# Kernel optimization log

Hardware: AMD Instinct MI355X
Metric: run time of the kernel (lower is better)

## Reference

```python
import math
import jax, jax.numpy as jnp
import numpy as np

B, D, COND, H, K, L, BOUND = 262144, 16, 8, 128, 10, 4, 1.0
D2 = math.ceil(D / 2)          # second split (spline-transformed channels) = 8
D1 = D - D2                    # passthrough channels = 8
DOUT = (3 * K + 1) * D2        # subnet output = 248
PMIN = 1e-3                    # BIN_WIDTH_MIN == BIN_HEIGHT_MIN == DELTA_MIN


def setup_inputs() -> dict:
    key = jax.random.key(0)
    ks = jax.random.split(key, 8)
    x = jax.random.normal(ks[0], (B, D), dtype=jnp.float32)
    c = jax.random.normal(ks[1], (B, COND), dtype=jnp.float32)
    din1 = D1 + COND
    W1s = jax.random.normal(ks[2], (L, din1, H), dtype=jnp.float32) * 0.1
    b1s = jnp.zeros((L, H), dtype=jnp.float32)
    Whs = jax.random.normal(ks[3], (L, H, H), dtype=jnp.float32) * 0.1
    bhs = jnp.zeros((L, H), dtype=jnp.float32)
    Wos = jax.random.normal(ks[4], (L, H, DOUT), dtype=jnp.float32) * 0.1
    bos = jnp.zeros((L, DOUT), dtype=jnp.float32)
    rng = np.random.default_rng(0)  # permutation_seed = 0
    perms = jnp.asarray(np.stack([rng.permutation(D) for _ in range(L)]), dtype=jnp.int32)
    return {"x": x, "c": c, "W1s": W1s, "b1s": b1s, "Whs": Whs, "bhs": bhs,
            "Wos": Wos, "bos": bos, "perms": perms}


def _softmax_with_min(t, m):
    return m + (1.0 - m * t.shape[-1]) * jax.nn.softmax(t, axis=-1)


def _unpack_theta(theta):
    # theta: [B, D2, 3K+1]
    bw_u, bh_u, ks_u = theta[..., :K], theta[..., K:2 * K], theta[..., 2 * K:]
    bin_w = 2.0 * BOUND * _softmax_with_min(bw_u, PMIN)
    bin_h = 2.0 * BOUND * _softmax_with_min(bh_u, PMIN)
    slopes = PMIN + (1.0 - PMIN) * jax.nn.softplus(ks_u) / math.log(2.0)
    pad = ((0, 0), (0, 0), (1, 0))
    x_knots = jnp.pad(jnp.cumsum(bin_w, axis=-1), pad) - BOUND
    y_knots = jnp.pad(jnp.cumsum(bin_h, axis=-1), pad) - BOUND
    return x_knots, y_knots, bin_w, bin_h, slopes


def _spline_fwd(x2, x_knots, y_knots, bin_w, bin_h, slopes):
    # x2: [B, D2]; knots: [B, D2, K+1]; widths/heights: [B, D2, K]; slopes: [B, D2, K+1]
    bin_idx = jnp.sum(x_knots < x2[..., None], axis=-1) - 1  # searchsorted(left) - 1
    in_bounds = (bin_idx >= 0) & (bin_idx < K)
    ci = jnp.clip(bin_idx, 0, K - 1)
    g = lambda t, i: jnp.take_along_axis(t, i[..., None], axis=-1)[..., 0]
    x1, y1 = g(x_knots, ci), g(y_knots, ci)
    xw, yw = g(bin_w, ci), g(bin_h, ci)
    d1, d2 = g(slopes, ci), g(slopes, ci + 1)
    # safe x so rational-quadratic never produces nan for masked-out lanes
    xs = jnp.where(in_bounds, x2, x1 + 0.5 * xw)
    s = yw / xw
    eta = (xs - x1) / xw
    rev_eta = 1.0 - eta
    err = eta * rev_eta
    y_denom = s + (d1 + d2 - 2.0 * s) * err
    y_rq = y1 + yw * (s * eta ** 2 + d1 * err) / y_denom
    jac_num = s ** 2 * (d2 * eta ** 2 + 2.0 * s * err + d1 * rev_eta ** 2)
    log_jac = jnp.log(jac_num) - 2.0 * jnp.log(y_denom)
    # out-of-bounds: linear extrapolation through the outermost knots
    xl, xr = x_knots[..., 0], x_knots[..., -1]
    yb, yt = y_knots[..., 0], y_knots[..., -1]
    y_lin = (yt - yb) / (xr - xl) * (x2 - xl) + yb
    yx = jnp.where(in_bounds, y_rq, y_lin)
    log_jac = jnp.where(in_bounds, log_jac, 0.0)
    return yx, jnp.sum(log_jac, axis=-1)


def _flow_forward(x, c, W1s, b1s, Whs, bhs, Wos, bos, perms):
    log_jac_det = jnp.zeros((x.shape[0],), dtype=x.dtype)
    for i in range(L):
        x1, x2 = x[:, :D1], x[:, D1:]
        h = jax.nn.relu(jnp.concatenate([x1, c], axis=1) @ W1s[i] + b1s[i])
        h = jax.nn.relu(h @ Whs[i] + bhs[i])
        theta = (h @ Wos[i] + bos[i]).reshape(-1, D2, 3 * K + 1)
        x_knots, y_knots, bin_w, bin_h, slopes = _unpack_theta(theta)
        y2, ljd = _spline_fwd(x2, x_knots, y_knots, bin_w, bin_h, slopes)
        log_jac_det = log_jac_det + ljd
        x_out = jnp.concatenate([x1, y2], axis=1)
        x = jnp.take(x_out, perms[i], axis=1)  # x @ channel_perm.T
    return x, log_jac_det


def reference(x, c, W1s, b1s, Whs, bhs, Wos, bos, perms):
    return _flow_forward(x, c, W1s, b1s, Whs, bhs, Wos, bos, perms)
```

## Files before the change

### kernel.cpp

```cpp
#include <hip/hip_runtime.h>

#define B_N   262144
#define PMIN_F 0.001f
#define LOG2E 1.44269504088896340736f
#define LN2   0.69314718055994530942f

typedef _Float16 half4v __attribute__((ext_vector_type(4)));
typedef _Float16 half8  __attribute__((ext_vector_type(8)));
typedef float    floatx4 __attribute__((ext_vector_type(4)));

__device__ __forceinline__ float fexp2(float x) { return __builtin_amdgcn_exp2f(x); }
__device__ __forceinline__ float flog2(float x) { return __builtin_amdgcn_logf(x); }
__device__ __forceinline__ float frcp (float x) { return __builtin_amdgcn_rcpf(x); }

__global__ __launch_bounds__(64) void prep_kernel(
    const float* __restrict__ W1s, const float* __restrict__ b1s,
    const float* __restrict__ Whs, const float* __restrict__ Wos,
    _Float16* __restrict__ ws)
{
    const int bid   = blockIdx.x;
    const int layer = bid / 104;
    const int r     = bid % 104;
    const int lane  = threadIdx.x;
    const int kg    = lane >> 4;
    const int c     = lane & 15;

    half8 v;
    if (r < 8) {
        const int nt = r, n = nt * 16 + c;
        const float* W1 = W1s + layer * 16 * 128;
        const float* b1 = b1s + layer * 128;
        #pragma unroll
        for (int j = 0; j < 8; ++j) {
            const int k = kg * 8 + j;
            v[j] = (k < 16) ? (_Float16)W1[k * 128 + n]
                 : (k == 16) ? (_Float16)b1[n] : (_Float16)0.f;
        }
    } else if (r < 40) {
        const int f = r - 8, nt = f >> 2, ks = f & 3, n = nt * 16 + c;
        const float* Wh = Whs + layer * 128 * 128;
        #pragma unroll
        for (int j = 0; j < 8; ++j) {
            const int k = ks * 32 + kg * 8 + j;
            v[j] = (_Float16)Wh[k * 128 + n];
        }
    } else {
        const int f = r - 40, nt = f >> 2, ks = f & 3, n = nt * 16 + c;
        const int dd = n >> 5, cc = n & 31;
        const float* Wo = Wos + layer * 128 * 248;
        #pragma unroll
        for (int j = 0; j < 8; ++j) {
            const int k = ks * 32 + kg * 8 + j;
            v[j] = (cc < 31) ? (_Float16)Wo[k * 248 + dd * 31 + cc] : (_Float16)0.f;
        }
    }
    *(half8*)(ws + (size_t)bid * 512 + lane * 8) = v;
}

__global__ __launch_bounds__(64, 3) void flow_mfma(
    const float* __restrict__ x_in,
    const float* __restrict__ c_in,
    const float* __restrict__ bhs,
    const float* __restrict__ bos,
    const int*   __restrict__ perms,
    const _Float16* __restrict__ wsW,
    float* __restrict__ out)
{
    __shared__ __align__(16) float    xls[2][256];
    __shared__ __align__(16) _Float16 R[2][2176];

    const int lane = threadIdx.x;
    const int q    = lane >> 4;
    const int m    = lane & 15;
    const long long row0 = (long long)blockIdx.x * 32;

    {
        const float4* xp = (const float4*)(x_in + row0 * 16);
        *(float4*)&xls[0][lane * 4] = xp[lane];
        *(float4*)&xls[1][lane * 4] = xp[lane + 64];
    }

    half8 a1c[2];
    #pragma unroll
    for (int t2 = 0; t2 < 2; ++t2) {
        #pragma unroll
        for (int j = 0; j < 8; ++j) a1c[t2][j] = (_Float16)0.f;
        if (q == 1) {
            const float4* cp = (const float4*)(c_in + (row0 + t2 * 16 + m) * 8);
            const float4 c0 = cp[0], c1 = cp[1];
            a1c[t2][0] = (_Float16)c0.x; a1c[t2][1] = (_Float16)c0.y;
            a1c[t2][2] = (_Float16)c0.z; a1c[t2][3] = (_Float16)c0.w;
            a1c[t2][4] = (_Float16)c1.x; a1c[t2][5] = (_Float16)c1.y;
            a1c[t2][6] = (_Float16)c1.z; a1c[t2][7] = (_Float16)c1.w;
        } else if (q == 2) {
            a1c[t2][0] = (_Float16)1.f;
        }
    }

    const int sp_t2  = lane >> 5;
    const int sp_row = (lane & 31) >> 1;
    const int sp_dl  = lane & 1;

    float ljacc = 0.f;

    for (int l = 0; l < 4; ++l) {
        const _Float16* wsl = wsW + (size_t)l * 104 * 512;
        const float* bh = bhs + l * 128;
        const float* bo = bos + l * 248;

        half8 a1[2];
        #pragma unroll
        for (int t2 = 0; t2 < 2; ++t2) {
            a1[t2] = a1c[t2];
            if (q == 0) {
                const float4 lo = *(const float4*)&xls[t2][m * 16];
                const float4 hi = *(const float4*)&xls[t2][m * 16 + 4];
                a1[t2][0] = (_Float16)lo.x; a1[t2][1] = (_Float16)lo.y;
                a1[t2][2] = (_Float16)lo.z; a1[t2][3] = (_Float16)lo.w;
                a1[t2][4] = (_Float16)hi.x; a1[t2][5] = (_Float16)hi.y;
                a1[t2][6] = (_Float16)hi.z; a1[t2][7] = (_Float16)hi.w;
            }
        }
        #pragma unroll
        for (int g = 0; g < 2; ++g) {
            const floatx4 z = {0.f, 0.f, 0.f, 0.f};
            floatx4 acc0[4], acc1[4];
            #pragma unroll
            for (int nt = 0; nt < 4; ++nt) {
                const half8 b = *(const half8*)(wsl + (g * 4 + nt) * 512 + lane * 8);
                acc0[nt] = __builtin_amdgcn_mfma_f32_16x16x32_f16(a1[0], b, z, 0, 0, 0);
                acc1[nt] = __builtin_amdgcn_mfma_f32_16x16x32_f16(a1[1], b, z, 0, 0, 0);
            }
            #pragma unroll
            for (int nt = 0; nt < 4; ++nt)
                #pragma unroll
                for (int reg = 0; reg < 4; ++reg) {
                    R[0][(q * 4 + reg) * 132 + (g * 4 + nt) * 16 + m] = (_Float16)fmaxf(acc0[nt][reg], 0.f);
                    R[1][(q * 4 + reg) * 132 + (g * 4 + nt) * 16 + m] = (_Float16)fmaxf(acc1[nt][reg], 0.f);
                }
        }

        half8 a2[2][4];
        #pragma unroll
        for (int t2 = 0; t2 < 2; ++t2)
            #pragma unroll
            for (int ks = 0; ks < 4; ++ks) {
                const half4v lo = *(const half4v*)&R[t2][m * 132 + ks * 32 + q * 8];
                const half4v hi = *(const half4v*)&R[t2][m * 132 + ks * 32 + q * 8 + 4];
                a2[t2][ks] = __builtin_shufflevector(lo, hi, 0, 1, 2, 3, 4, 5, 6, 7);
            }
        #pragma unroll
        for (int g = 0; g < 2; ++g) {
            floatx4 acc0[4], acc1[4];
            #pragma unroll
            for (int nt = 0; nt < 4; ++nt) {
                const float bb = bh[(g * 4 + nt) * 16 + m];
                acc0[nt][0] = bb; acc0[nt][1] = bb; acc0[nt][2] = bb; acc0[nt][3] = bb;
                acc1[nt] = acc0[nt];
            }
            #pragma unroll
            for (int ks = 0; ks < 4; ++ks)
                #pragma unroll
                for (int nt = 0; nt < 4; ++nt) {
                    const half8 b = *(const half8*)(wsl + (8 + (g * 4 + nt) * 4 + ks) * 512 + lane * 8);
                    acc0[nt] = __builtin_amdgcn_mfma_f32_16x16x32_f16(a2[0][ks], b, acc0[nt], 0, 0, 0);
                    acc1[nt] = __builtin_amdgcn_mfma_f32_16x16x32_f16(a2[1][ks], b, acc1[nt], 0, 0, 0);
                }
            #pragma unroll
            for (int nt = 0; nt < 4; ++nt)
                #pragma unroll
                for (int reg = 0; reg < 4; ++reg) {
                    R[0][(q * 4 + reg) * 132 + (g * 4 + nt) * 16 + m] = (_Float16)fmaxf(acc0[nt][reg], 0.f);
                    R[1][(q * 4 + reg) * 132 + (g * 4 + nt) * 16 + m] = (_Float16)fmaxf(acc1[nt][reg], 0.f);
                }
        }

        half8 a3[2][4];
        #pragma unroll
        for (int t2 = 0; t2 < 2; ++t2)
            #pragma unroll
            for (int ks = 0; ks < 4; ++ks) {
                const half4v lo = *(const half4v*)&R[t2][m * 132 + ks * 32 + q * 8];
                const half4v hi = *(const half4v*)&R[t2][m * 132 + ks * 32 + q * 8 + 4];
                a3[t2][ks] = __builtin_shufflevector(lo, hi, 0, 1, 2, 3, 4, 5, 6, 7);
            }
        __syncthreads();

        float* Rf0 = (float*)&R[0][0];
        float* Rf1 = (float*)&R[1][0];

        #pragma unroll
        for (int qd = 0; qd < 4; ++qd) {
            {
                floatx4 acc0[4], acc1[4];
                #pragma unroll
                for (int j = 0; j < 4; ++j) {
                    const int n = qd * 64 + j * 16 + m;
                    const int cc = n & 31;
                    const float bb = (cc < 31) ? bo[(n >> 5) * 31 + cc] : 0.f;
                    acc0[j][0] = bb; acc0[j][1] = bb; acc0[j][2] = bb; acc0[j][3] = bb;
                    acc1[j] = acc0[j];
                }
                #pragma unroll
                for (int ks = 0; ks < 4; ++ks)
                    #pragma unroll
                    for (int j = 0; j < 4; ++j) {
                        const int nt = qd * 4 + j;
                        const half8 b = *(const half8*)(wsl + (40 + nt * 4 + ks) * 512 + lane * 8);
                        acc0[j] = __builtin_amdgcn_mfma_f32_16x16x32_f16(a3[0][ks], b, acc0[j], 0, 0, 0);
                        acc1[j] = __builtin_amdgcn_mfma_f32_16x16x32_f16(a3[1][ks], b, acc1[j], 0, 0, 0);
                    }
                #pragma unroll
                for (int j = 0; j < 4; ++j) {
                    const int off = (j >> 1) * 32 + (j & 1) * 16 + m;
                    #pragma unroll
                    for (int reg = 0; reg < 4; ++reg) {
                        Rf0[(q * 4 + reg) * 68 + off] = acc0[j][reg];
                        Rf1[(q * 4 + reg) * 68 + off] = acc1[j][reg];
                    }
                }
            }

            {
                const int d    = qd * 2 + sp_dl;
                const int base = sp_row * 68 + sp_dl * 32;
                const float* Rf = sp_t2 ? Rf1 : Rf0;

                const float4 v0 = *(const float4*)&Rf[base];
                const float4 v1 = *(const float4*)&Rf[base + 4];
                const float4 v2 = *(const float4*)&Rf[base + 8];
                const float4 v3 = *(const float4*)&Rf[base + 12];
                const float4 v4 = *(const float4*)&Rf[base + 16];
                const float x2 = xls[sp_t2][sp_row * 16 + 8 + d];

                float tw[10] = {v0.x, v0.y, v0.z, v0.w, v1.x, v1.y, v1.z, v1.w, v2.x, v2.y};
                float m1 = tw[0];
                #pragma unroll
                for (int i = 1; i < 10; ++i) m1 = fmaxf(m1, tw[i]);
                float se = 0.f;
                #pragma unroll
                for (int i = 0; i < 10; ++i) { tw[i] = fexp2((tw[i] - m1) * LOG2E); se += tw[i]; }
                const float inv198 = 1.98f * frcp(se);

                int cnt = 0;
                {
                    float run = -1.f;
                    cnt += (run < x2) ? 1 : 0;
                    #pragma unroll
                    for (int i = 0; i < 10; ++i) {
                        run = run + fmaf(tw[i], inv198, 0.002f);
                        cnt += (run < x2) ? 1 : 0;
                    }
                }
                const int bidx = cnt - 1;
                const bool inb = (bidx >= 0) && (bidx < 10);
                const int ci = bidx < 0 ? 0 : (bidx > 9 ? 9 : bidx);

                float xlo = -1.f, xhi = 0.f, rx;
                {
                    float run = -1.f;
                    #pragma unroll
                    for (int i = 0; i < 10; ++i) {
                        const bool pick = (i == ci);
                        xlo = pick ? run : xlo;
                        run = run + fmaf(tw[i], inv198, 0.002f);
                        xhi = pick ? run : xhi;
                    }
                    rx = run;
                }

                float hh[10] = {v2.z, v2.w, v3.x, v3.y, v3.z, v3.w, v4.x, v4.y, v4.z, v4.w};
                float hm = hh[0];
                #pragma unroll
                for (int i = 1; i < 10; ++i) hm = fmaxf(hm, hh[i]);
                float seh = 0.f;
                #pragma unroll
                for (int i = 0; i < 10; ++i) { hh[i] = fexp2((hh[i] - hm) * LOG2E); seh += hh[i]; }
                const float invh = 1.98f * frcp(seh);
                float ylo = -1.f, yhi = 0.f, ry;
                {
                    float run = -1.f;
                    #pragma unroll
                    for (int i = 0; i < 10; ++i) {
                        const bool pick = (i == ci);
                        ylo = pick ? run : ylo;
                        run = run + fmaf(hh[i], invh, 0.002f);
                        yhi = pick ? run : yhi;
                    }
                    ry = run;
                }

                const float xw = xhi - xlo, yw = yhi - ylo;

                const float u1 = Rf[base + 20 + ci];
                const float u2 = Rf[base + 21 + ci];
                const float t1 = u1 * LOG2E;
                const float t2s = u2 * LOG2E;
                const float dd1 = PMIN_F + 0.999f * ((t1  > 15.f) ? t1  : flog2(1.f + fexp2(t1)));
                const float dd2 = PMIN_F + 0.999f * ((t2s > 15.f) ? t2s : flog2(1.f + fexp2(t2s)));

                const float xs  = inb ? x2 : (xlo + 0.5f * xw);
                const float rxw = frcp(xw);
                const float s   = yw * rxw;
                const float eta = (xs - xlo) * rxw;
                const float rev = 1.f - eta;
                const float er  = eta * rev;
                const float dn  = s + (dd1 + dd2 - 2.f * s) * er;
                const float yrq = ylo + yw * (s * eta * eta + dd1 * er) * frcp(dn);
                const float jn  = s * s * (dd2 * eta * eta + 2.f * s * er + dd1 * rev * rev);
                const float ljx = LN2 * (flog2(jn) - 2.f * flog2(dn));
                const float ylin = (ry + 1.f) * frcp(rx + 1.f) * (x2 + 1.f) - 1.f;

                xls[sp_t2][sp_row * 16 + 8 + d] = inb ? yrq : ylin;
                ljacc += inb ? ljx : 0.f;
            }
        }

        {
            const int4 pv = ((const int4*)(perms + l * 16))[lane & 3];
            const int mm = lane >> 2;
            const float a0 = xls[0][mm * 16 + pv.x];
            const float a1v = xls[0][mm * 16 + pv.y];
            const float a2v = xls[0][mm * 16 + pv.z];
            const float a3v = xls[0][mm * 16 + pv.w];
            const float b0 = xls[1][mm * 16 + pv.x];
            const float b1v = xls[1][mm * 16 + pv.y];
            const float b2 = xls[1][mm * 16 + pv.z];
            const float b3 = xls[1][mm * 16 + pv.w];
            *(float4*)&xls[0][lane * 4] = make_float4(a0, a1v, a2v, a3v);
            *(float4*)&xls[1][lane * 4] = make_float4(b0, b1v, b2, b3);
        }
        __syncthreads();
    }

    #pragma unroll
    for (int t2 = 0; t2 < 2; ++t2) {
        const float4 vo = *(const float4*)&xls[t2][lane * 4];
        ((float4*)(out + (row0 + t2 * 16) * 16))[lane] = vo;
    }
    {
        const float ljs = ljacc + __shfl_xor(ljacc, 1);
        if ((lane & 1) == 0)
            out[(size_t)B_N * 16 + row0 + sp_t2 * 16 + sp_row] = ljs;
    }
}

extern "C" void kernel_launch(void* const* d_in, const int* in_sizes, int n_in,
                              void* d_out, int out_size, void* d_ws, size_t ws_size,
                              hipStream_t stream) {
    const float* x     = (const float*)d_in[0];
    const float* c     = (const float*)d_in[1];
    const float* W1s   = (const float*)d_in[2];
    const float* b1s   = (const float*)d_in[3];
    const float* Whs   = (const float*)d_in[4];
    const float* bhs   = (const float*)d_in[5];
    const float* Wos   = (const float*)d_in[6];
    const float* bos   = (const float*)d_in[7];
    const int*   perms = (const int*)d_in[8];
    float* out = (float*)d_out;
    _Float16* ws = (_Float16*)d_ws;

    prep_kernel<<<dim3(416), dim3(64), 0, stream>>>(W1s, b1s, Whs, Wos, ws);
    flow_mfma<<<dim3(B_N / 32), dim3(64), 0, stream>>>(
        x, c, bhs, bos, perms, ws, out);
}
```

Baseline: 280.4 us.

## Process 64 rows per wavefront to reuse weight fragments across four M-tiles

Each single-wave block now handles four 16-row tiles instead of two, so every weight B-fragment loaded from global memory feeds four MFMAs rather than two. This halves the weight-load traffic per row and the grid size. The spline evaluation moves into a helper and each lane runs it twice per quarter. In exchange, accumulator and A-fragment register use roughly doubles, so launch bounds drop to two waves per SIMD and shared memory per block doubles, which lowers occupancy and the ability to hide latency.

```diff
diff --git a/kernel.cpp b/kernel.cpp
--- a/kernel.cpp
+++ b/kernel.cpp
@@ -57,7 +57,98 @@
     *(half8*)(ws + (size_t)bid * 512 + lane * 8) = v;
 }
 
-__global__ __launch_bounds__(64, 3) void flow_mfma(
+__device__ __forceinline__ void spline_eval(const float* __restrict__ Rf, const int base,
+                                            const float x2, float& yout, float& ljout)
+{
+    const float4 v0 = *(const float4*)&Rf[base];
+    const float4 v1 = *(const float4*)&Rf[base + 4];
+    const float4 v2 = *(const float4*)&Rf[base + 8];
+    const float4 v3 = *(const float4*)&Rf[base + 12];
+    const float4 v4 = *(const float4*)&Rf[base + 16];
+
+    float tw[10] = {v0.x, v0.y, v0.z, v0.w, v1.x, v1.y, v1.z, v1.w, v2.x, v2.y};
+    float m1 = tw[0];
+    #pragma unroll
+    for (int i = 1; i < 10; ++i) m1 = fmaxf(m1, tw[i]);
+    float se = 0.f;
+    #pragma unroll
+    for (int i = 0; i < 10; ++i) { tw[i] = fexp2((tw[i] - m1) * LOG2E); se += tw[i]; }
+    const float inv198 = 1.98f * frcp(se);
+
+    int cnt = 0;
+    {
+        float run = -1.f;
+        cnt += (run < x2) ? 1 : 0;
+        #pragma unroll
+        for (int i = 0; i < 10; ++i) {
+            run = run + fmaf(tw[i], inv198, 0.002f);
+            cnt += (run < x2) ? 1 : 0;
+        }
+    }
+    const int bidx = cnt - 1;
+    const bool inb = (bidx >= 0) && (bidx < 10);
+    const int ci = bidx < 0 ? 0 : (bidx > 9 ? 9 : bidx);
+
+    float xlo = -1.f, xhi = 0.f, rx;
+    {
+        float run = -1.f;
+        #pragma unroll
+        for (int i = 0; i < 10; ++i) {
+            const bool pick = (i == ci);
+            xlo = pick ? run : xlo;
+            run = run + fmaf(tw[i], inv198, 0.002f);
+            xhi = pick ? run : xhi;
+        }
+        rx = run;
+    }
+
+    float hh[10] = {v2.z, v2.w, v3.x, v3.y, v3.z, v3.w, v4.x, v4.y, v4.z, v4.w};
+    float hm = hh[0];
+    #pragma unroll
+    for (int i = 1; i < 10; ++i) hm = fmaxf(hm, hh[i]);
+    float seh = 0.f;
+    #pragma unroll
+    for (int i = 0; i < 10; ++i) { hh[i] = fexp2((hh[i] - hm) * LOG2E); seh += hh[i]; }
+    const float invh = 1.98f * frcp(seh);
+    float ylo = -1.f, yhi = 0.f, ry;
+    {
+        float run = -1.f;
+        #pragma unroll
+        for (int i = 0; i < 10; ++i) {
+            const bool pick = (i == ci);
+            ylo = pick ? run : ylo;
+            run = run + fmaf(hh[i], invh, 0.002f);
+            yhi = pick ? run : yhi;
+        }
+        ry = run;
+    }
+
+    const float xw = xhi - xlo, yw = yhi - ylo;
+
+    const float u1 = Rf[base + 20 + ci];
+    const float u2 = Rf[base + 21 + ci];
+    const float t1 = u1 * LOG2E;
+    const float t2s = u2 * LOG2E;
+    const float dd1 = PMIN_F + 0.999f * ((t1  > 15.f) ? t1  : flog2(1.f + fexp2(t1)));
+    const float dd2 = PMIN_F + 0.999f * ((t2s > 15.f) ? t2s : flog2(1.f + fexp2(t2s)));
+
+    const float xs  = inb ? x2 : (xlo + 0.5f * xw);
+    const float rxw = frcp(xw);
+    const float s   = yw * rxw;
+    const float eta = (xs - xlo) * rxw;
+    const float rev = 1.f - eta;
+    const float er  = eta * rev;
+    const float dn  = s + (dd1 + dd2 - 2.f * s) * er;
+    const float yrq = ylo + yw * (s * eta * eta + dd1 * er) * frcp(dn);
+    const float jn  = s * s * (dd2 * eta * eta + 2.f * s * er + dd1 * rev * rev);
+    const float ljx = LN2 * (flog2(jn) - 2.f * flog2(dn));
+    const float ylin = (ry + 1.f) * frcp(rx + 1.f) * (x2 + 1.f) - 1.f;
+
+    yout  = inb ? yrq : ylin;
+    ljout = inb ? ljx : 0.f;
+}
+
+__global__ __launch_bounds__(64, 2) void flow_mfma(
     const float* __restrict__ x_in,
     const float* __restrict__ c_in,
     const float* __restrict__ bhs,
@@ -66,140 +157,148 @@
     const _Float16* __restrict__ wsW,
     float* __restrict__ out)
 {
-    __shared__ __align__(16) float    xls[2][256];
-    __shared__ __align__(16) _Float16 R[2][2176];
+    __shared__ __align__(16) float    xls[4][256];
+    __shared__ __align__(16) _Float16 R[4][2176];
 
     const int lane = threadIdx.x;
     const int q    = lane >> 4;
     const int m    = lane & 15;
-    const long long row0 = (long long)blockIdx.x * 32;
+    const long long row0 = (long long)blockIdx.x * 64;
 
     {
         const float4* xp = (const float4*)(x_in + row0 * 16);
-        *(float4*)&xls[0][lane * 4] = xp[lane];
-        *(float4*)&xls[1][lane * 4] = xp[lane + 64];
-    }
-
-    half8 a1c[2];
-    #pragma unroll
-    for (int t2 = 0; t2 < 2; ++t2) {
-        #pragma unroll
-        for (int j = 0; j < 8; ++j) a1c[t2][j] = (_Float16)0.f;
+        #pragma unroll
+        for (int t = 0; t < 4; ++t)
+            *(float4*)&xls[t][lane * 4] = xp[lane + t * 64];
+    }
+
+    half8 a1c[4];
+    #pragma unroll
+    for (int t = 0; t < 4; ++t) {
+        #pragma unroll
+        for (int j = 0; j < 8; ++j) a1c[t][j] = (_Float16)0.f;
         if (q == 1) {
-            const float4* cp = (const float4*)(c_in + (row0 + t2 * 16 + m) * 8);
+            const float4* cp = (const float4*)(c_in + (row0 + t * 16 + m) * 8);
             const float4 c0 = cp[0], c1 = cp[1];
-            a1c[t2][0] = (_Float16)c0.x; a1c[t2][1] = (_Float16)c0.y;
-            a1c[t2][2] = (_Float16)c0.z; a1c[t2][3] = (_Float16)c0.w;
-            a1c[t2][4] = (_Float16)c1.x; a1c[t2][5] = (_Float16)c1.y;
-            a1c[t2][6] = (_Float16)c1.z; a1c[t2][7] = (_Float16)c1.w;
+            a1c[t][0] = (_Float16)c0.x; a1c[t][1] = (_Float16)c0.y;
+            a1c[t][2] = (_Float16)c0.z; a1c[t][3] = (_Float16)c0.w;
+            a1c[t][4] = (_Float16)c1.x; a1c[t][5] = (_Float16)c1.y;
+            a1c[t][6] = (_Float16)c1.z; a1c[t][7] = (_Float16)c1.w;
         } else if (q == 2) {
-            a1c[t2][0] = (_Float16)1.f;
-        }
-    }
-
-    const int sp_t2  = lane >> 5;
+            a1c[t][0] = (_Float16)1.f;
+        }
+    }
+
+    const int sp_ta  = lane >> 5;
     const int sp_row = (lane & 31) >> 1;
     const int sp_dl  = lane & 1;
 
-    float ljacc = 0.f;
+    float ljA = 0.f, ljB = 0.f;
 
     for (int l = 0; l < 4; ++l) {
         const _Float16* wsl = wsW + (size_t)l * 104 * 512;
         const float* bh = bhs + l * 128;
         const float* bo = bos + l * 248;
 
-        half8 a1[2];
-        #pragma unroll
-        for (int t2 = 0; t2 < 2; ++t2) {
-            a1[t2] = a1c[t2];
+        half8 a1[4];
+        #pragma unroll
+        for (int t = 0; t < 4; ++t) {
+            a1[t] = a1c[t];
             if (q == 0) {
-                const float4 lo = *(const float4*)&xls[t2][m * 16];
-                const float4 hi = *(const float4*)&xls[t2][m * 16 + 4];
-                a1[t2][0] = (_Float16)lo.x; a1[t2][1] = (_Float16)lo.y;
-                a1[t2][2] = (_Float16)lo.z; a1[t2][3] = (_Float16)lo.w;
-                a1[t2][4] = (_Float16)hi.x; a1[t2][5] = (_Float16)hi.y;
-                a1[t2][6] = (_Float16)hi.z; a1[t2][7] = (_Float16)hi.w;
+                const float4 lo = *(const float4*)&xls[t][m * 16];
+                const float4 hi = *(const float4*)&xls[t][m * 16 + 4];
+                a1[t][0] = (_Float16)lo.x; a1[t][1] = (_Float16)lo.y;
+                a1[t][2] = (_Float16)lo.z; a1[t][3] = (_Float16)lo.w;
+                a1[t][4] = (_Float16)hi.x; a1[t][5] = (_Float16)hi.y;
+                a1[t][6] = (_Float16)hi.z; a1[t][7] = (_Float16)hi.w;
             }
         }
         #pragma unroll
         for (int g = 0; g < 2; ++g) {
             const floatx4 z = {0.f, 0.f, 0.f, 0.f};
-            floatx4 acc0[4], acc1[4];
+            floatx4 acc[4][4];
             #pragma unroll
             for (int nt = 0; nt < 4; ++nt) {
                 const half8 b = *(const half8*)(wsl + (g * 4 + nt) * 512 + lane * 8);
-                acc0[nt] = __builtin_amdgcn_mfma_f32_16x16x32_f16(a1[0], b, z, 0, 0, 0);
-                acc1[nt] = __builtin_amdgcn_mfma_f32_16x16x32_f16(a1[1], b, z, 0, 0, 0);
+                #pragma unroll
+                for (int t = 0; t < 4; ++t)
+                    acc[t][nt] = __builtin_amdgcn_mfma_f32_16x16x32_f16(a1[t], b, z, 0, 0, 0);
             }
             #pragma unroll
             for (int nt = 0; nt < 4; ++nt)
                 #pragma unroll
-                for (int reg = 0; reg < 4; ++reg) {
-                    R[0][(q * 4 + reg) * 132 + (g * 4 + nt) * 16 + m] = (_Float16)fmaxf(acc0[nt][reg], 0.f);
-                    R[1][(q * 4 + reg) * 132 + (g * 4 + nt) * 16 + m] = (_Float16)fmaxf(acc1[nt][reg], 0.f);
-                }
-        }
-
-        half8 a2[2][4];
-        #pragma unroll
-        for (int t2 = 0; t2 < 2; ++t2)
+                for (int reg = 0; reg < 4; ++reg)
+                    #pragma unroll
+                    for (int t = 0; t < 4; ++t)
+                        R[t][(q * 4 + reg) * 132 + (g * 4 + nt) * 16 + m] =
+                            (_Float16)fmaxf(acc[t][nt][reg], 0.f);
+        }
+
+        half8 a2[4][4];
+        #pragma unroll
+        for (int t = 0; t < 4; ++t)
             #pragma unroll
             for (int ks = 0; ks < 4; ++ks) {
-                const half4v lo = *(const half4v*)&R[t2][m * 132 + ks * 32 + q * 8];
-                const half4v hi = *(const half4v*)&R[t2][m * 132 + ks * 32 + q * 8 + 4];
-                a2[t2][ks] = __builtin_shufflevector(lo, hi, 0, 1, 2, 3, 4, 5, 6, 7);
+                const half4v lo = *(const half4v*)&R[t][m * 132 + ks * 32 + q * 8];
+                const half4v hi = *(const half4v*)&R[t][m * 132 + ks * 32 + q * 8 + 4];
+                a2[t][ks] = __builtin_shufflevector(lo, hi, 0, 1, 2, 3, 4, 5, 6, 7);
             }
         #pragma unroll
         for (int g = 0; g < 2; ++g) {
-            floatx4 acc0[4], acc1[4];
+            floatx4 acc[4][4];
             #pragma unroll
             for (int nt = 0; nt < 4; ++nt) {
                 const float bb = bh[(g * 4 + nt) * 16 + m];
-                acc0[nt][0] = bb; acc0[nt][1] = bb; acc0[nt][2] = bb; acc0[nt][3] = bb;
-                acc1[nt] = acc0[nt];
+                #pragma unroll
+                for (int t = 0; t < 4; ++t) {
+                    acc[t][nt][0] = bb; acc[t][nt][1] = bb;
+                    acc[t][nt][2] = bb; acc[t][nt][3] = bb;
+                }
             }
             #pragma unroll
             for (int ks = 0; ks < 4; ++ks)
                 #pragma unroll
                 for (int nt = 0; nt < 4; ++nt) {
                     const half8 b = *(const half8*)(wsl + (8 + (g * 4 + nt) * 4 + ks) * 512 + lane * 8);
-                    acc0[nt] = __builtin_amdgcn_mfma_f32_16x16x32_f16(a2[0][ks], b, acc0[nt], 0, 0, 0);
-                    acc1[nt] = __builtin_amdgcn_mfma_f32_16x16x32_f16(a2[1][ks], b, acc1[nt], 0, 0, 0);
+                    #pragma unroll
+                    for (int t = 0; t < 4; ++t)
+                        acc[t][nt] = __builtin_amdgcn_mfma_f32_16x16x32_f16(a2[t][ks], b, acc[t][nt], 0, 0, 0);
                 }
             #pragma unroll
             for (int nt = 0; nt < 4; ++nt)
                 #pragma unroll
-                for (int reg = 0; reg < 4; ++reg) {
-                    R[0][(q * 4 + reg) * 132 + (g * 4 + nt) * 16 + m] = (_Float16)fmaxf(acc0[nt][reg], 0.f);
-                    R[1][(q * 4 + reg) * 132 + (g * 4 + nt) * 16 + m] = (_Float16)fmaxf(acc1[nt][reg], 0.f);
-                }
-        }
-
-        half8 a3[2][4];
-        #pragma unroll
-        for (int t2 = 0; t2 < 2; ++t2)
+                for (int reg = 0; reg < 4; ++reg)
+                    #pragma unroll
+                    for (int t = 0; t < 4; ++t)
+                        R[t][(q * 4 + reg) * 132 + (g * 4 + nt) * 16 + m] =
+                            (_Float16)fmaxf(acc[t][nt][reg], 0.f);
+        }
+
+        half8 a3[4][4];
+        #pragma unroll
+        for (int t = 0; t < 4; ++t)
             #pragma unroll
             for (int ks = 0; ks < 4; ++ks) {
-                const half4v lo = *(const half4v*)&R[t2][m * 132 + ks * 32 + q * 8];
-                const half4v hi = *(const half4v*)&R[t2][m * 132 + ks * 32 + q * 8 + 4];
-                a3[t2][ks] = __builtin_shufflevector(lo, hi, 0, 1, 2, 3, 4, 5, 6, 7);
+                const half4v lo = *(const half4v*)&R[t][m * 132 + ks * 32 + q * 8];
+                const half4v hi = *(const half4v*)&R[t][m * 132 + ks * 32 + q * 8 + 4];
+                a3[t][ks] = __builtin_shufflevector(lo, hi, 0, 1, 2, 3, 4, 5, 6, 7);
             }
         __syncthreads();
-
-        float* Rf0 = (float*)&R[0][0];
-        float* Rf1 = (float*)&R[1][0];
 
         #pragma unroll
         for (int qd = 0; qd < 4; ++qd) {
             {
-                floatx4 acc0[4], acc1[4];
+                floatx4 acc[4][4];
                 #pragma unroll
                 for (int j = 0; j < 4; ++j) {
                     const int n = qd * 64 + j * 16 + m;
                     const int cc = n & 31;
                     const float bb = (cc < 31) ? bo[(n >> 5) * 31 + cc] : 0.f;
-                    acc0[j][0] = bb; acc0[j][1] = bb; acc0[j][2] = bb; acc0[j][3] = bb;
-                    acc1[j] = acc0[j];
+                    #pragma unroll
+                    for (int t = 0; t < 4; ++t) {
+                        acc[t][j][0] = bb; acc[t][j][1] = bb;
+                        acc[t][j][2] = bb; acc[t][j][3] = bb;
+                    }
                 }
                 #pragma unroll
                 for (int ks = 0; ks < 4; ++ks)
@@ -207,141 +306,64 @@
                     for (int j = 0; j < 4; ++j) {
                         const int nt = qd * 4 + j;
                         const half8 b = *(const half8*)(wsl + (40 + nt * 4 + ks) * 512 + lane * 8);
-                        acc0[j] = __builtin_amdgcn_mfma_f32_16x16x32_f16(a3[0][ks], b, acc0[j], 0, 0, 0);
-                        acc1[j] = __builtin_amdgcn_mfma_f32_16x16x32_f16(a3[1][ks], b, acc1[j], 0, 0, 0);
+                        #pragma unroll
+                        for (int t = 0; t < 4; ++t)
+                            acc[t][j] = __builtin_amdgcn_mfma_f32_16x16x32_f16(a3[t][ks], b, acc[t][j], 0, 0, 0);
                     }
                 #pragma unroll
                 for (int j = 0; j < 4; ++j) {
                     const int off = (j >> 1) * 32 + (j & 1) * 16 + m;
                     #pragma unroll
-                    for (int reg = 0; reg < 4; ++reg) {
-                        Rf0[(q * 4 + reg) * 68 + off] = acc0[j][reg];
-                        Rf1[(q * 4 + reg) * 68 + off] = acc1[j][reg];
-                    }
+                    for (int reg = 0; reg < 4; ++reg)
+                        #pragma unroll
+                        for (int t = 0; t < 4; ++t)
+                            ((float*)&R[t][0])[(q * 4 + reg) * 68 + off] = acc[t][j][reg];
                 }
             }
 
             {
                 const int d    = qd * 2 + sp_dl;
                 const int base = sp_row * 68 + sp_dl * 32;
-                const float* Rf = sp_t2 ? Rf1 : Rf0;
-
-                const float4 v0 = *(const float4*)&Rf[base];
-                const float4 v1 = *(const float4*)&Rf[base + 4];
-                const float4 v2 = *(const float4*)&Rf[base + 8];
-                const float4 v3 = *(const float4*)&Rf[base + 12];
-                const float4 v4 = *(const float4*)&Rf[base + 16];
-                const float x2 = xls[sp_t2][sp_row * 16 + 8 + d];
-
-                float tw[10] = {v0.x, v0.y, v0.z, v0.w, v1.x, v1.y, v1.z, v1.w, v2.x, v2.y};
-                float m1 = tw[0];
-                #pragma unroll
-                for (int i = 1; i < 10; ++i) m1 = fmaxf(m1, tw[i]);
-                float se = 0.f;
-                #pragma unroll
-                for (int i = 0; i < 10; ++i) { tw[i] = fexp2((tw[i] - m1) * LOG2E); se += tw[i]; }
-                const float inv198 = 1.98f * frcp(se);
-
-                int cnt = 0;
-                {
-                    float run = -1.f;
-                    cnt += (run < x2) ? 1 : 0;
-                    #pragma unroll
-                    for (int i = 0; i < 10; ++i) {
-                        run = run + fmaf(tw[i], inv198, 0.002f);
-                        cnt += (run < x2) ? 1 : 0;
-                    }
-                }
-                const int bidx = cnt - 1;
-                const bool inb = (bidx >= 0) && (bidx < 10);
-                const int ci = bidx < 0 ? 0 : (bidx > 9 ? 9 : bidx);
-
-                float xlo = -1.f, xhi = 0.f, rx;
-                {
-                    float run = -1.f;
-                    #pragma unroll
-                    for (int i = 0; i < 10; ++i) {
-                        const bool pick = (i == ci);
-                        xlo = pick ? run : xlo;
-                        run = run + fmaf(tw[i], inv198, 0.002f);
-                        xhi = pick ? run : xhi;
-                    }
-                    rx = run;
-                }
-
-                float hh[10] = {v2.z, v2.w, v3.x, v3.y, v3.z, v3.w, v4.x, v4.y, v4.z, v4.w};
-                float hm = hh[0];
-                #pragma unroll
-                for (int i = 1; i < 10; ++i) hm = fmaxf(hm, hh[i]);
-                float seh = 0.f;
-                #pragma unroll
-                for (int i = 0; i < 10; ++i) { hh[i] = fexp2((hh[i] - hm) * LOG2E); seh += hh[i]; }
-                const float invh = 1.98f * frcp(seh);
-                float ylo = -1.f, yhi = 0.f, ry;
-                {
-                    float run = -1.f;
-                    #pragma unroll
-                    for (int i = 0; i < 10; ++i) {
-                        const bool pick = (i == ci);
-                        ylo = pick ? run : ylo;
-                        run = run + fmaf(hh[i], invh, 0.002f);
-                        yhi = pick ? run : yhi;
-                    }
-                    ry = run;
-                }
-
-                const float xw = xhi - xlo, yw = yhi - ylo;
-
-                const float u1 = Rf[base + 20 + ci];
-                const float u2 = Rf[base + 21 + ci];
-                const float t1 = u1 * LOG2E;
-                const float t2s = u2 * LOG2E;
-                const float dd1 = PMIN_F + 0.999f * ((t1  > 15.f) ? t1  : flog2(1.f + fexp2(t1)));
-                const float dd2 = PMIN_F + 0.999f * ((t2s > 15.f) ? t2s : flog2(1.f + fexp2(t2s)));
-
-                const float xs  = inb ? x2 : (xlo + 0.5f * xw);
-                const float rxw = frcp(xw);
-                const float s   = yw * rxw;
-                const float eta = (xs - xlo) * rxw;
-                const float rev = 1.f - eta;
-                const float er  = eta * rev;
-                const float dn  = s + (dd1 + dd2 - 2.f * s) * er;
-                const float yrq = ylo + yw * (s * eta * eta + dd1 * er) * frcp(dn);
-                const float jn  = s * s * (dd2 * eta * eta + 2.f * s * er + dd1 * rev * rev);
-                const float ljx = LN2 * (flog2(jn) - 2.f * flog2(dn));
-                const float ylin = (ry + 1.f) * frcp(rx + 1.f) * (x2 + 1.f) - 1.f;
-
-                xls[sp_t2][sp_row * 16 + 8 + d] = inb ? yrq : ylin;
-                ljacc += inb ? ljx : 0.f;
+                const int xi   = sp_row * 16 + 8 + d;
+
+                float yA, lA, yB, lB;
+                spline_eval((const float*)&R[sp_ta][0],     base, xls[sp_ta][xi],     yA, lA);
+                spline_eval((const float*)&R[sp_ta + 2][0], base, xls[sp_ta + 2][xi], yB, lB);
+
+                xls[sp_ta][xi]     = yA;
+                xls[sp_ta + 2][xi] = yB;
+                ljA += lA;
+                ljB += lB;
             }
         }
 
         {
             const int4 pv = ((const int4*)(perms + l * 16))[lane & 3];
             const int mm = lane >> 2;
-            const float a0 = xls[0][mm * 16 + pv.x];
-            const float a1v = xls[0][mm * 16 + pv.y];
-            const float a2v = xls[0][mm * 16 + pv.z];
-            const float a3v = xls[0][mm * 16 + pv.w];
-            const float b0 = xls[1][mm * 16 + pv.x];
-            const float b1v = xls[1][mm * 16 + pv.y];
-            const float b2 = xls[1][mm * 16 + pv.z];
-            const float b3 = xls[1][mm * 16 + pv.w];
-            *(float4*)&xls[0][lane * 4] = make_float4(a0, a1v, a2v, a3v);
-            *(float4*)&xls[1][lane * 4] = make_float4(b0, b1v, b2, b3);
+            #pragma unroll
+            for (int t = 0; t < 4; ++t) {
+                const float a0  = xls[t][mm * 16 + pv.x];
+                const float a1v = xls[t][mm * 16 + pv.y];
+                const float a2v = xls[t][mm * 16 + pv.z];
+                const float a3v = xls[t][mm * 16 + pv.w];
+                *(float4*)&xls[t][lane * 4] = make_float4(a0, a1v, a2v, a3v);
+            }
         }
         __syncthreads();
     }
 
     #pragma unroll
-    for (int t2 = 0; t2 < 2; ++t2) {
-        const float4 vo = *(const float4*)&xls[t2][lane * 4];
-        ((float4*)(out + (row0 + t2 * 16) * 16))[lane] = vo;
-    }
-    {
-        const float ljs = ljacc + __shfl_xor(ljacc, 1);
-        if ((lane & 1) == 0)
-            out[(size_t)B_N * 16 + row0 + sp_t2 * 16 + sp_row] = ljs;
+    for (int t = 0; t < 4; ++t) {
+        const float4 vo = *(const float4*)&xls[t][lane * 4];
+        ((float4*)(out + (row0 + t * 16) * 16))[lane] = vo;
+    }
+    {
+        const float sA = ljA + __shfl_xor(ljA, 1);
+        const float sB = ljB + __shfl_xor(ljB, 1);
+        if ((lane & 1) == 0) {
+            out[(size_t)B_N * 16 + row0 + sp_ta * 16 + sp_row]       = sA;
+            out[(size_t)B_N * 16 + row0 + (sp_ta + 2) * 16 + sp_row] = sB;
+        }
     }
 }
 
@@ -361,6 +383,6 @@
     _Float16* ws = (_Float16*)d_ws;
 
     prep_kernel<<<dim3(416), dim3(64), 0, stream>>>(W1s, b1s, Whs, Wos, ws);
-    flow_mfma<<<dim3(B_N / 32), dim3(64), 0, stream>>>(
+    flow_mfma<<<dim3(B_N / 64), dim3(64), 0, stream>>>(
         x, c, bhs, bos, perms, ws, out);
 }
```

After: 346.7 us. +23.6%, slower.

## Cut register pressure to raise occupancy to four waves per EU

Applied to the files above, without the earlier changes.

Replaces launch_bounds min-blocks 3 with amdgpu_waves_per_eu(4) and reduces live registers so more waves fit. The hoisted conditioning-input fragment is now rebuilt from global memory every layer instead of being kept in registers. MFMA loops now process two N-tiles at a time instead of four, so fewer accumulators are live. The spline code moves into a helper that defers the height loads. The aim is more waves to hide latency, at the cost of reloading c each layer and possible spills or lost instruction-level parallelism.

```diff
diff --git a/kernel.cpp b/kernel.cpp
--- a/kernel.cpp
+++ b/kernel.cpp
@@ -57,7 +57,100 @@
     *(half8*)(ws + (size_t)bid * 512 + lane * 8) = v;
 }
 
-__global__ __launch_bounds__(64, 3) void flow_mfma(
+__device__ __forceinline__ void spline_eval(const float* __restrict__ Rf, const int base,
+                                            const float x2, float& yout, float& ljout)
+{
+    const float4 v0 = *(const float4*)&Rf[base];
+    const float4 v1 = *(const float4*)&Rf[base + 4];
+    const float4 v2 = *(const float4*)&Rf[base + 8];
+
+    float tw[10] = {v0.x, v0.y, v0.z, v0.w, v1.x, v1.y, v1.z, v1.w, v2.x, v2.y};
+    float m1 = tw[0];
+    #pragma unroll
+    for (int i = 1; i < 10; ++i) m1 = fmaxf(m1, tw[i]);
+    float se = 0.f;
+    #pragma unroll
+    for (int i = 0; i < 10; ++i) { tw[i] = fexp2((tw[i] - m1) * LOG2E); se += tw[i]; }
+    const float inv198 = 1.98f * frcp(se);
+
+    int cnt = 0;
+    {
+        float run = -1.f;
+        cnt += (run < x2) ? 1 : 0;
+        #pragma unroll
+        for (int i = 0; i < 10; ++i) {
+            run = run + fmaf(tw[i], inv198, 0.002f);
+            cnt += (run < x2) ? 1 : 0;
+        }
+    }
+    const int bidx = cnt - 1;
+    const bool inb = (bidx >= 0) && (bidx < 10);
+    const int ci = bidx < 0 ? 0 : (bidx > 9 ? 9 : bidx);
+
+    float xlo = -1.f, xhi = 0.f, rx;
+    {
+        float run = -1.f;
+        #pragma unroll
+        for (int i = 0; i < 10; ++i) {
+            const bool pick = (i == ci);
+            xlo = pick ? run : xlo;
+            run = run + fmaf(tw[i], inv198, 0.002f);
+            xhi = pick ? run : xhi;
+        }
+        rx = run;
+    }
+
+    const float4 v3 = *(const float4*)&Rf[base + 12];
+    const float4 v4 = *(const float4*)&Rf[base + 16];
+
+    float hh[10] = {v2.z, v2.w, v3.x, v3.y, v3.z, v3.w, v4.x, v4.y, v4.z, v4.w};
+    float hm = hh[0];
+    #pragma unroll
+    for (int i = 1; i < 10; ++i) hm = fmaxf(hm, hh[i]);
+    float seh = 0.f;
+    #pragma unroll
+    for (int i = 0; i < 10; ++i) { hh[i] = fexp2((hh[i] - hm) * LOG2E); seh += hh[i]; }
+    const float invh = 1.98f * frcp(seh);
+    float ylo = -1.f, yhi = 0.f, ry;
+    {
+        float run = -1.f;
+        #pragma unroll
+        for (int i = 0; i < 10; ++i) {
+            const bool pick = (i == ci);
+            ylo = pick ? run : ylo;
+            run = run + fmaf(hh[i], invh, 0.002f);
+            yhi = pick ? run : yhi;
+        }
+        ry = run;
+    }
+
+    const float xw = xhi - xlo, yw = yhi - ylo;
+
+    const float u1 = Rf[base + 20 + ci];
+    const float u2 = Rf[base + 21 + ci];
+    const float t1 = u1 * LOG2E;
+    const float t2s = u2 * LOG2E;
+    const float dd1 = PMIN_F + 0.999f * ((t1  > 15.f) ? t1  : flog2(1.f + fexp2(t1)));
+    const float dd2 = PMIN_F + 0.999f * ((t2s > 15.f) ? t2s : flog2(1.f + fexp2(t2s)));
+
+    const float xs  = inb ? x2 : (xlo + 0.5f * xw);
+    const float rxw = frcp(xw);
+    const float s   = yw * rxw;
+    const float eta = (xs - xlo) * rxw;
+    const float rev = 1.f - eta;
+    const float er  = eta * rev;
+    const float dn  = s + (dd1 + dd2 - 2.f * s) * er;
+    const float yrq = ylo + yw * (s * eta * eta + dd1 * er) * frcp(dn);
+    const float jn  = s * s * (dd2 * eta * eta + 2.f * s * er + dd1 * rev * rev);
+    const float ljx = LN2 * (flog2(jn) - 2.f * flog2(dn));
+    const float ylin = (ry + 1.f) * frcp(rx + 1.f) * (x2 + 1.f) - 1.f;
+
+    yout  = inb ? yrq : ylin;
+    ljout = inb ? ljx : 0.f;
+}
+
+__global__ __attribute__((amdgpu_waves_per_eu(4))) __launch_bounds__(64)
+void flow_mfma(
     const float* __restrict__ x_in,
     const float* __restrict__ c_in,
     const float* __restrict__ bhs,
@@ -80,23 +173,6 @@
         *(float4*)&xls[1][lane * 4] = xp[lane + 64];
     }
 
-    half8 a1c[2];
-    #pragma unroll
-    for (int t2 = 0; t2 < 2; ++t2) {
-        #pragma unroll
-        for (int j = 0; j < 8; ++j) a1c[t2][j] = (_Float16)0.f;
-        if (q == 1) {
-            const float4* cp = (const float4*)(c_in + (row0 + t2 * 16 + m) * 8);
-            const float4 c0 = cp[0], c1 = cp[1];
-            a1c[t2][0] = (_Float16)c0.x; a1c[t2][1] = (_Float16)c0.y;
-            a1c[t2][2] = (_Float16)c0.z; a1c[t2][3] = (_Float16)c0.w;
-            a1c[t2][4] = (_Float16)c1.x; a1c[t2][5] = (_Float16)c1.y;
-            a1c[t2][6] = (_Float16)c1.z; a1c[t2][7] = (_Float16)c1.w;
-        } else if (q == 2) {
-            a1c[t2][0] = (_Float16)1.f;
-        }
-    }
-
     const int sp_t2  = lane >> 5;
     const int sp_row = (lane & 31) >> 1;
     const int sp_dl  = lane & 1;
@@ -111,7 +187,8 @@
         half8 a1[2];
         #pragma unroll
         for (int t2 = 0; t2 < 2; ++t2) {
-            a1[t2] = a1c[t2];
+            #pragma unroll
+            for (int j = 0; j < 8; ++j) a1[t2][j] = (_Float16)0.f;
             if (q == 0) {
                 const float4 lo = *(const float4*)&xls[t2][m * 16];
                 const float4 hi = *(const float4*)&xls[t2][m * 16 + 4];
@@ -119,26 +196,38 @@
                 a1[t2][2] = (_Float16)lo.z; a1[t2][3] = (_Float16)lo.w;
                 a1[t2][4] = (_Float16)hi.x; a1[t2][5] = (_Float16)hi.y;
                 a1[t2][6] = (_Float16)hi.z; a1[t2][7] = (_Float16)hi.w;
-            }
-        }
-        #pragma unroll
-        for (int g = 0; g < 2; ++g) {
-            const floatx4 z = {0.f, 0.f, 0.f, 0.f};
-            floatx4 acc0[4], acc1[4];
-            #pragma unroll
-            for (int nt = 0; nt < 4; ++nt) {
-                const half8 b = *(const half8*)(wsl + (g * 4 + nt) * 512 + lane * 8);
-                acc0[nt] = __builtin_amdgcn_mfma_f32_16x16x32_f16(a1[0], b, z, 0, 0, 0);
-                acc1[nt] = __builtin_amdgcn_mfma_f32_16x16x32_f16(a1[1], b, z, 0, 0, 0);
-            }
-            #pragma unroll
-            for (int nt = 0; nt < 4; ++nt)
+            } else if (q == 1) {
+                const float4* cp = (const float4*)(c_in + (row0 + t2 * 16 + m) * 8);
+                const float4 c0 = cp[0], c1 = cp[1];
+                a1[t2][0] = (_Float16)c0.x; a1[t2][1] = (_Float16)c0.y;
+                a1[t2][2] = (_Float16)c0.z; a1[t2][3] = (_Float16)c0.w;
+                a1[t2][4] = (_Float16)c1.x; a1[t2][5] = (_Float16)c1.y;
+                a1[t2][6] = (_Float16)c1.z; a1[t2][7] = (_Float16)c1.w;
+            } else if (q == 2) {
+                a1[t2][0] = (_Float16)1.f;
+            }
+        }
+
+        #pragma unroll
+        for (int g = 0; g < 2; ++g)
+            #pragma unroll
+            for (int p = 0; p < 2; ++p) {
+                const int nt0 = g * 4 + p * 2, nt1 = nt0 + 1;
+                const floatx4 z = {0.f, 0.f, 0.f, 0.f};
+                const half8 b0 = *(const half8*)(wsl + nt0 * 512 + lane * 8);
+                const half8 b1 = *(const half8*)(wsl + nt1 * 512 + lane * 8);
+                floatx4 acc00 = __builtin_amdgcn_mfma_f32_16x16x32_f16(a1[0], b0, z, 0, 0, 0);
+                floatx4 acc01 = __builtin_amdgcn_mfma_f32_16x16x32_f16(a1[1], b0, z, 0, 0, 0);
+                floatx4 acc10 = __builtin_amdgcn_mfma_f32_16x16x32_f16(a1[0], b1, z, 0, 0, 0);
+                floatx4 acc11 = __builtin_amdgcn_mfma_f32_16x16x32_f16(a1[1], b1, z, 0, 0, 0);
                 #pragma unroll
                 for (int reg = 0; reg < 4; ++reg) {
-                    R[0][(q * 4 + reg) * 132 + (g * 4 + nt) * 16 + m] = (_Float16)fmaxf(acc0[nt][reg], 0.f);
-                    R[1][(q * 4 + reg) * 132 + (g * 4 + nt) * 16 + m] = (_Float16)fmaxf(acc1[nt][reg], 0.f);
-                }
-        }
+                    R[0][(q * 4 + reg) * 132 + nt0 * 16 + m] = (_Float16)fmaxf(acc00[reg], 0.f);
+                    R[1][(q * 4 + reg) * 132 + nt0 * 16 + m] = (_Float16)fmaxf(acc01[reg], 0.f);
+                    R[0][(q * 4 + reg) * 132 + nt1 * 16 + m] = (_Float16)fmaxf(acc10[reg], 0.f);
+                    R[1][(q * 4 + reg) * 132 + nt1 * 16 + m] = (_Float16)fmaxf(acc11[reg], 0.f);
+                }
+            }
 
         half8 a2[2][4];
         #pragma unroll
@@ -149,31 +238,38 @@
                 const half4v hi = *(const half4v*)&R[t2][m * 132 + ks * 32 + q * 8 + 4];
                 a2[t2][ks] = __builtin_shufflevector(lo, hi, 0, 1, 2, 3, 4, 5, 6, 7);
             }
-        #pragma unroll
-        for (int g = 0; g < 2; ++g) {
-            floatx4 acc0[4], acc1[4];
-            #pragma unroll
-            for (int nt = 0; nt < 4; ++nt) {
-                const float bb = bh[(g * 4 + nt) * 16 + m];
-                acc0[nt][0] = bb; acc0[nt][1] = bb; acc0[nt][2] = bb; acc0[nt][3] = bb;
-                acc1[nt] = acc0[nt];
-            }
-            #pragma unroll
-            for (int ks = 0; ks < 4; ++ks)
+
+        #pragma unroll
+        for (int g = 0; g < 2; ++g)
+            #pragma unroll
+            for (int p = 0; p < 2; ++p) {
+                const int nt0 = g * 4 + p * 2, nt1 = nt0 + 1;
+                floatx4 acc00, acc01, acc10, acc11;
+                {
+                    const float bb0 = bh[nt0 * 16 + m];
+                    const float bb1 = bh[nt1 * 16 + m];
+                    acc00[0] = bb0; acc00[1] = bb0; acc00[2] = bb0; acc00[3] = bb0;
+                    acc01 = acc00;
+                    acc10[0] = bb1; acc10[1] = bb1; acc10[2] = bb1; acc10[3] = bb1;
+                    acc11 = acc10;
+                }
                 #pragma unroll
-                for (int nt = 0; nt < 4; ++nt) {
-                    const half8 b = *(const half8*)(wsl + (8 + (g * 4 + nt) * 4 + ks) * 512 + lane * 8);
-                    acc0[nt] = __builtin_amdgcn_mfma_f32_16x16x32_f16(a2[0][ks], b, acc0[nt], 0, 0, 0);
-                    acc1[nt] = __builtin_amdgcn_mfma_f32_16x16x32_f16(a2[1][ks], b, acc1[nt], 0, 0, 0);
-                }
-            #pragma unroll
-            for (int nt = 0; nt < 4; ++nt)
+                for (int ks = 0; ks < 4; ++ks) {
+                    const half8 b0 = *(const half8*)(wsl + (8 + nt0 * 4 + ks) * 512 + lane * 8);
+                    const half8 b1 = *(const half8*)(wsl + (8 + nt1 * 4 + ks) * 512 + lane * 8);
+                    acc00 = __builtin_amdgcn_mfma_f32_16x16x32_f16(a2[0][ks], b0, acc00, 0, 0, 0);
+                    acc01 = __builtin_amdgcn_mfma_f32_16x16x32_f16(a2[1][ks], b0, acc01, 0, 0, 0);
+                    acc10 = __builtin_amdgcn_mfma_f32_16x16x32_f16(a2[0][ks], b1, acc10, 0, 0, 0);
+                    acc11 = __builtin_amdgcn_mfma_f32_16x16x32_f16(a2[1][ks], b1, acc11, 0, 0, 0);
+                }
                 #pragma unroll
                 for (int reg = 0; reg < 4; ++reg) {
-                    R[0][(q * 4 + reg) * 132 + (g * 4 + nt) * 16 + m] = (_Float16)fmaxf(acc0[nt][reg], 0.f);
-                    R[1][(q * 4 + reg) * 132 + (g * 4 + nt) * 16 + m] = (_Float16)fmaxf(acc1[nt][reg], 0.f);
-                }
-        }
+                    R[0][(q * 4 + reg) * 132 + nt0 * 16 + m] = (_Float16)fmaxf(acc00[reg], 0.f);
+                    R[1][(q * 4 + reg) * 132 + nt0 * 16 + m] = (_Float16)fmaxf(acc01[reg], 0.f);
+                    R[0][(q * 4 + reg) * 132 + nt1 * 16 + m] = (_Float16)fmaxf(acc10[reg], 0.f);
+                    R[1][(q * 4 + reg) * 132 + nt1 * 16 + m] = (_Float16)fmaxf(acc11[reg], 0.f);
+                }
+            }
 
         half8 a3[2][4];
         #pragma unroll
@@ -191,32 +287,40 @@
 
         #pragma unroll
         for (int qd = 0; qd < 4; ++qd) {
-            {
-                floatx4 acc0[4], acc1[4];
+            #pragma unroll
+            for (int p = 0; p < 2; ++p) {
+                const int j0 = p * 2, j1 = j0 + 1;
+                floatx4 acc00, acc01, acc10, acc11;
+                {
+                    const int n0 = qd * 64 + j0 * 16 + m;
+                    const int n1 = qd * 64 + j1 * 16 + m;
+                    const int cc0 = n0 & 31, cc1 = n1 & 31;
+                    const float bb0 = (cc0 < 31) ? bo[(n0 >> 5) * 31 + cc0] : 0.f;
+                    const float bb1 = (cc1 < 31) ? bo[(n1 >> 5) * 31 + cc1] : 0.f;
+                    acc00[0] = bb0; acc00[1] = bb0; acc00[2] = bb0; acc00[3] = bb0;
+                    acc01 = acc00;
+                    acc10[0] = bb1; acc10[1] = bb1; acc10[2] = bb1; acc10[3] = bb1;
+                    acc11 = acc10;
+                }
                 #pragma unroll
-                for (int j = 0; j < 4; ++j) {
-                    const int n = qd * 64 + j * 16 + m;
-                    const int cc = n & 31;
-                    const float bb = (cc < 31) ? bo[(n >> 5) * 31 + cc] : 0.f;
-                    acc0[j][0] = bb; acc0[j][1] = bb; acc0[j][2] = bb; acc0[j][3] = bb;
-                    acc1[j] = acc0[j];
-                }
-                #pragma unroll
-                for (int ks = 0; ks < 4; ++ks)
-                    #pragma unroll
-                    for (int j = 0; j < 4; ++j) {
-                        const int nt = qd * 4 + j;
-                        const half8 b = *(const half8*)(wsl + (40 + nt * 4 + ks) * 512 + lane * 8);
-                        acc0[j] = __builtin_amdgcn_mfma_f32_16x16x32_f16(a3[0][ks], b, acc0[j], 0, 0, 0);
-                        acc1[j] = __builtin_amdgcn_mfma_f32_16x16x32_f16(a3[1][ks], b, acc1[j], 0, 0, 0);
-                    }
-                #pragma unroll
-                for (int j = 0; j < 4; ++j) {
-                    const int off = (j >> 1) * 32 + (j & 1) * 16 + m;
+                for (int ks = 0; ks < 4; ++ks) {
+                    const int nt0 = qd * 4 + j0, nt1 = qd * 4 + j1;
+                    const half8 b0 = *(const half8*)(wsl + (40 + nt0 * 4 + ks) * 512 + lane * 8);
+                    const half8 b1 = *(const half8*)(wsl + (40 + nt1 * 4 + ks) * 512 + lane * 8);
+                    acc00 = __builtin_amdgcn_mfma_f32_16x16x32_f16(a3[0][ks], b0, acc00, 0, 0, 0);
+                    acc01 = __builtin_amdgcn_mfma_f32_16x16x32_f16(a3[1][ks], b0, acc01, 0, 0, 0);
+                    acc10 = __builtin_amdgcn_mfma_f32_16x16x32_f16(a3[0][ks], b1, acc10, 0, 0, 0);
+                    acc11 = __builtin_amdgcn_mfma_f32_16x16x32_f16(a3[1][ks], b1, acc11, 0, 0, 0);
+                }
+                {
+                    const int off0 = (j0 >> 1) * 32 + (j0 & 1) * 16 + m;
+                    const int off1 = (j1 >> 1) * 32 + (j1 & 1) * 16 + m;
                     #pragma unroll
                     for (int reg = 0; reg < 4; ++reg) {
-                        Rf0[(q * 4 + reg) * 68 + off] = acc0[j][reg];
-                        Rf1[(q * 4 + reg) * 68 + off] = acc1[j][reg];
+                        Rf0[(q * 4 + reg) * 68 + off0] = acc00[reg];
+                        Rf1[(q * 4 + reg) * 68 + off0] = acc01[reg];
+                        Rf0[(q * 4 + reg) * 68 + off1] = acc10[reg];
+                        Rf1[(q * 4 + reg) * 68 + off1] = acc11[reg];
                     }
                 }
             }
@@ -225,94 +329,12 @@
                 const int d    = qd * 2 + sp_dl;
                 const int base = sp_row * 68 + sp_dl * 32;
                 const float* Rf = sp_t2 ? Rf1 : Rf0;
-
-                const float4 v0 = *(const float4*)&Rf[base];
-                const float4 v1 = *(const float4*)&Rf[base + 4];
-                const float4 v2 = *(const float4*)&Rf[base + 8];
-                const float4 v3 = *(const float4*)&Rf[base + 12];
-                const float4 v4 = *(const float4*)&Rf[base + 16];
-                const float x2 = xls[sp_t2][sp_row * 16 + 8 + d];
-
-                float tw[10] = {v0.x, v0.y, v0.z, v0.w, v1.x, v1.y, v1.z, v1.w, v2.x, v2.y};
-                float m1 = tw[0];
-                #pragma unroll
-                for (int i = 1; i < 10; ++i) m1 = fmaxf(m1, tw[i]);
-                float se = 0.f;
-                #pragma unroll
-                for (int i = 0; i < 10; ++i) { tw[i] = fexp2((tw[i] - m1) * LOG2E); se += tw[i]; }
-                const float inv198 = 1.98f * frcp(se);
-
-                int cnt = 0;
-                {
-                    float run = -1.f;
-                    cnt += (run < x2) ? 1 : 0;
-                    #pragma unroll
-                    for (int i = 0; i < 10; ++i) {
-                        run = run + fmaf(tw[i], inv198, 0.002f);
-                        cnt += (run < x2) ? 1 : 0;
-                    }
-                }
-                const int bidx = cnt - 1;
-                const bool inb = (bidx >= 0) && (bidx < 10);
-                const int ci = bidx < 0 ? 0 : (bidx > 9 ? 9 : bidx);
-
-                float xlo = -1.f, xhi = 0.f, rx;
-                {
-                    float run = -1.f;
-                    #pragma unroll
-                    for (int i = 0; i < 10; ++i) {
-                        const bool pick = (i == ci);
-                        xlo = pick ? run : xlo;
-                        run = run + fmaf(tw[i], inv198, 0.002f);
-                        xhi = pick ? run : xhi;
-                    }
-                    rx = run;
-                }
-
-                float hh[10] = {v2.z, v2.w, v3.x, v3.y, v3.z, v3.w, v4.x, v4.y, v4.z, v4.w};
-                float hm = hh[0];
-                #pragma unroll
-                for (int i = 1; i < 10; ++i) hm = fmaxf(hm, hh[i]);
-                float seh = 0.f;
-                #pragma unroll
-                for (int i = 0; i < 10; ++i) { hh[i] = fexp2((hh[i] - hm) * LOG2E); seh += hh[i]; }
-                const float invh = 1.98f * frcp(seh);
-                float ylo = -1.f, yhi = 0.f, ry;
-                {
-                    float run = -1.f;
-                    #pragma unroll
-                    for (int i = 0; i < 10; ++i) {
-                        const bool pick = (i == ci);
-                        ylo = pick ? run : ylo;
-                        run = run + fmaf(hh[i], invh, 0.002f);
-                        yhi = pick ? run : yhi;
-                    }
-                    ry = run;
-                }
-
-                const float xw = xhi - xlo, yw = yhi - ylo;
-
-                const float u1 = Rf[base + 20 + ci];
-                const float u2 = Rf[base + 21 + ci];
-                const float t1 = u1 * LOG2E;
-                const float t2s = u2 * LOG2E;
-                const float dd1 = PMIN_F + 0.999f * ((t1  > 15.f) ? t1  : flog2(1.f + fexp2(t1)));
-                const float dd2 = PMIN_F + 0.999f * ((t2s > 15.f) ? t2s : flog2(1.f + fexp2(t2s)));
-
-                const float xs  = inb ? x2 : (xlo + 0.5f * xw);
-                const float rxw = frcp(xw);
-                const float s   = yw * rxw;
-                const float eta = (xs - xlo) * rxw;
-                const float rev = 1.f - eta;
-                const float er  = eta * rev;
-                const float dn  = s + (dd1 + dd2 - 2.f * s) * er;
-                const float yrq = ylo + yw * (s * eta * eta + dd1 * er) * frcp(dn);
-                const float jn  = s * s * (dd2 * eta * eta + 2.f * s * er + dd1 * rev * rev);
-                const float ljx = LN2 * (flog2(jn) - 2.f * flog2(dn));
-                const float ylin = (ry + 1.f) * frcp(rx + 1.f) * (x2 + 1.f) - 1.f;
-
-                xls[sp_t2][sp_row * 16 + 8 + d] = inb ? yrq : ylin;
-                ljacc += inb ? ljx : 0.f;
+                const int xi   = sp_row * 16 + 8 + d;
+
+                float yv, lj;
+                spline_eval(Rf, base, xls[sp_t2][xi], yv, lj);
+                xls[sp_t2][xi] = yv;
+                ljacc += lj;
             }
         }
 
```

Measured after the change: 290.4 us. +3.6%, slower.
